# Kernel tuning notes

Hardware: AMD Instinct MI355X
Metric: run time of the kernel (lower is better)

The kernel has to match this reference:

```python
import jax, jax.numpy as jnp
import numpy as np
import math

S, B, D = 2048, 2, 1024
H = 16
DH = D // H
WIN = 256
DIL = 1


def setup_inputs() -> dict:
    key = jax.random.key(0)
    ks = jax.random.split(key, 10)
    std = 1.0 / math.sqrt(D)
    return {
        "x": jax.random.normal(ks[0], (S, B, D), jnp.float32),
        "beta": jax.random.normal(ks[1], (H,), jnp.float32) * 0.02,
        "Wq": jax.random.normal(ks[2], (D, D), jnp.float32) * std,
        "bq": jnp.zeros((D,), jnp.float32),
        "Wk": jax.random.normal(ks[3], (D, D), jnp.float32) * std,
        "bk": jnp.zeros((D,), jnp.float32),
        "Wv": jax.random.normal(ks[4], (D, D), jnp.float32) * std,
        "bv": jnp.zeros((D,), jnp.float32),
        "Wo": jax.random.normal(ks[5], (D, D), jnp.float32) * std,
        "bo": jnp.zeros((D,), jnp.float32),
    }


def _split_heads(t):
    # (S, B, D) -> (B*H, S, DH), matching rearrange 's b (h d) -> (b h) s d'
    return t.reshape(S, B, H, DH).transpose(1, 2, 0, 3).reshape(B * H, S, DH)


def reference(x, beta, Wq, bq, Wk, bk, Wv, bv, Wo, bo):
    q = _split_heads(x @ Wq + bq)
    k = _split_heads(x @ Wk + bk)
    v = _split_heads(x @ Wv + bv)

    # per-head learnable temperature: q / (sqrt(d_head) * exp(beta))
    beta_exp = jnp.tile(jnp.exp(beta), B)  # (B*H,), head index = z % H
    q = q / (jnp.sqrt(jnp.asarray(DH, x.dtype)) * beta_exp)[:, None, None]

    # causal dilated windowed mask
    idx = jnp.arange(S)
    diff = idx[:, None] - idx[None, :]
    allowed = (diff >= 0) & (diff <= DIL * (WIN - 1)) & (diff % DIL == 0)
    mask = jnp.where(allowed, jnp.asarray(0.0, x.dtype), jnp.asarray(-jnp.inf, x.dtype))

    scores = jnp.einsum('zqd,zkd->zqk', q, k) + mask[None]
    # attention sink: extra zero-logit column absorbing probability mass
    scores = jnp.concatenate([scores, jnp.zeros((B * H, S, 1), scores.dtype)], axis=-1)
    attn = jax.nn.softmax(scores, axis=-1)[..., :-1]

    out = jnp.einsum('zqk,zkd->zqd', attn, v)
    # (B*H, S, DH) -> (S, B, D)
    out = out.reshape(B, H, S, DH).transpose(2, 0, 1, 3).reshape(S, B, D)
    return out @ Wo + bo
```

## Files before the change

### kernel.cpp

```cpp
#include <hip/hip_runtime.h>
#include <math.h>

#define S_LEN  2048
#define BATCH  2
#define DM     1024
#define NHEAD  16
#define DHEAD  64
#define WIN    256
#define MROWS  4096

#define KP   72
#define PPAD 68

#define BM 256
#define BN 192
#define BK 64

typedef __attribute__((ext_vector_type(8))) short bf16x8;
typedef __attribute__((ext_vector_type(4))) float f32x4;

__device__ __forceinline__ unsigned short f2b(float f) {
    unsigned int u = __float_as_uint(f);
    return (unsigned short)((u + 0x7fffu + ((u >> 16) & 1u)) >> 16);
}
__device__ __forceinline__ void gld16(const void* g, void* l) {
    __builtin_amdgcn_global_load_lds(
        (const __attribute__((address_space(1))) void*)g,
        (__attribute__((address_space(3))) void*)l, 16, 0, 0);
}
__device__ __forceinline__ bf16x8 pack8(float4 a, float4 b) {
    bf16x8 r;
    r[0] = (short)f2b(a.x); r[1] = (short)f2b(a.y);
    r[2] = (short)f2b(a.z); r[3] = (short)f2b(a.w);
    r[4] = (short)f2b(b.x); r[5] = (short)f2b(b.y);
    r[6] = (short)f2b(b.z); r[7] = (short)f2b(b.w);
    return r;
}

__global__ __launch_bounds__(256)
void cvtx(const float* __restrict__ x, unsigned short* __restrict__ xb)
{
    const int i = (blockIdx.x * 256 + threadIdx.x) * 4;
    float4 f = *(const float4*)(x + i);
    ushort4 o; o.x = f2b(f.x); o.y = f2b(f.y); o.z = f2b(f.z); o.w = f2b(f.w);
    *(ushort4*)(xb + i) = o;
}

__global__ __launch_bounds__(256)
void twcvt4(const float* __restrict__ W0, const float* __restrict__ W1,
            const float* __restrict__ W2, const float* __restrict__ W3,
            unsigned short* __restrict__ T0, unsigned short* __restrict__ T1,
            unsigned short* __restrict__ T2, unsigned short* __restrict__ T3)
{
    const int zz = blockIdx.z;
    const float* W = (zz == 0) ? W0 : (zz == 1) ? W1 : (zz == 2) ? W2 : W3;
    unsigned short* WT = (zz == 0) ? T0 : (zz == 1) ? T1 : (zz == 2) ? T2 : T3;

    __shared__ float t32[32][33];
    const int bx = blockIdx.x * 32;
    const int by = blockIdx.y * 32;
    const int c  = threadIdx.x & 31;
    const int r0 = threadIdx.x >> 5;
#pragma unroll
    for (int p = 0; p < 4; ++p)
        t32[r0 + 8 * p][c] = W[(size_t)(by + r0 + 8 * p) * DM + bx + c];
    __syncthreads();
#pragma unroll
    for (int p = 0; p < 4; ++p)
        WT[(size_t)(bx + r0 + 8 * p) * DM + by + c] = f2b(t32[c][r0 + 8 * p]);
}

__global__ __launch_bounds__(512, 2)
void gemm_qkv(const unsigned short* __restrict__ A,
              const unsigned short* __restrict__ BT,
              const float* __restrict__ b0,
              const float* __restrict__ b1,
              const float* __restrict__ b2,
              const float* __restrict__ beta,
              unsigned short* __restrict__ Cb)
{
    __shared__ unsigned short Ab[2][BM * BK];
    __shared__ unsigned short Bb[2][BN * BK];

    const int t   = threadIdx.x;
    const int ln  = t & 63;
    const int wv  = t >> 6;
    const int wr  = wv >> 2;
    const int wc  = wv & 3;
    const int m16 = ln & 15;
    const int g   = ln >> 4;
    const int sw  = m16 & 7;

    const int rowBase = blockIdx.y * BM;
    const int colBase = blockIdx.x * BN;

    const int sr  = t >> 3;
    const int scx = (t & 7) ^ (sr & 7);
    const size_t gOff = (size_t)sr * DM + scx * 8;
    const int    ldOff = t * 8;

    f32x4 acc[8][3];
#pragma unroll
    for (int u = 0; u < 8; ++u)
#pragma unroll
        for (int v = 0; v < 3; ++v)
            acc[u][v] = (f32x4){0.f, 0.f, 0.f, 0.f};

    {
        const unsigned short* a0 = A  + (size_t)rowBase * DM + gOff;
        const unsigned short* bt = BT + (size_t)colBase * DM + gOff;
#pragma unroll
        for (int cb = 0; cb < 3; ++cb)
            gld16(bt + (size_t)cb * 64 * DM, &Bb[0][cb * 4096 + ldOff]);
#pragma unroll
        for (int ca = 0; ca < 4; ++ca)
            gld16(a0 + (size_t)ca * 64 * DM, &Ab[0][ca * 4096 + ldOff]);
        asm volatile("s_waitcnt vmcnt(0)" ::: "memory");
        __builtin_amdgcn_s_barrier();
    }

    bf16x8 af[4][2], bfr[2][2];

    for (int kt = 0; kt < DM / BK; ++kt) {
        const int cur = kt & 1;
        const unsigned short* Ac = Ab[cur];
        const unsigned short* Bc = Bb[cur];
        unsigned short* An = Ab[cur ^ 1];
        unsigned short* Bn = Bb[cur ^ 1];
        const bool hn = (kt < DM / BK - 1);
        const unsigned short* aS = A  + (size_t)rowBase * DM + (kt + 1) * BK + gOff;
        const unsigned short* bS = BT + (size_t)colBase * DM + (kt + 1) * BK + gOff;

#pragma unroll
        for (int u = 0; u < 4; ++u) {
            const int ro = (wr * 128 + u * 16 + m16) * BK;
#pragma unroll
            for (int kk = 0; kk < 2; ++kk)
                af[u][kk] = *(const bf16x8*)&Ac[ro + (((kk << 2) | g) ^ sw) * 8];
        }
#pragma unroll
        for (int v = 0; v < 2; ++v) {
            const int ro = (wc * 48 + v * 16 + m16) * BK;
#pragma unroll
            for (int kk = 0; kk < 2; ++kk)
                bfr[v][kk] = *(const bf16x8*)&Bc[ro + (((kk << 2) | g) ^ sw) * 8];
        }
        if (hn) {
            gld16(bS,                      &Bn[ldOff]);
            gld16(bS + (size_t)64 * DM,    &Bn[4096 + ldOff]);
        }
        __builtin_amdgcn_s_barrier();
        __builtin_amdgcn_s_setprio(1);
#pragma unroll
        for (int u = 0; u < 4; ++u)
#pragma unroll
            for (int v = 0; v < 2; ++v) {
                acc[u][v] = __builtin_amdgcn_mfma_f32_16x16x32_bf16(
                    af[u][0], bfr[v][0], acc[u][v], 0, 0, 0);
                acc[u][v] = __builtin_amdgcn_mfma_f32_16x16x32_bf16(
                    af[u][1], bfr[v][1], acc[u][v], 0, 0, 0);
            }
        __builtin_amdgcn_s_setprio(0);
        __builtin_amdgcn_s_barrier();

        {
            const int ro = (wc * 48 + 32 + m16) * BK;
#pragma unroll
            for (int kk = 0; kk < 2; ++kk)
                bfr[0][kk] = *(const bf16x8*)&Bc[ro + (((kk << 2) | g) ^ sw) * 8];
        }
        if (hn) {
            gld16(bS + (size_t)128 * DM,   &Bn[2 * 4096 + ldOff]);
            gld16(aS,                      &An[ldOff]);
        }
        __builtin_amdgcn_s_barrier();
        __builtin_amdgcn_s_setprio(1);
#pragma unroll
        for (int u = 0; u < 4; ++u) {
            acc[u][2] = __builtin_amdgcn_mfma_f32_16x16x32_bf16(
                af[u][0], bfr[0][0], acc[u][2], 0, 0, 0);
            acc[u][2] = __builtin_amdgcn_mfma_f32_16x16x32_bf16(
                af[u][1], bfr[0][1], acc[u][2], 0, 0, 0);
        }
        __builtin_amdgcn_s_setprio(0);
        asm volatile("s_waitcnt vmcnt(4)" ::: "memory");
        __builtin_amdgcn_s_barrier();

#pragma unroll
        for (int u = 0; u < 4; ++u) {
            const int ro = (wr * 128 + 64 + u * 16 + m16) * BK;
#pragma unroll
            for (int kk = 0; kk < 2; ++kk)
                af[u][kk] = *(const bf16x8*)&Ac[ro + (((kk << 2) | g) ^ sw) * 8];
        }
#pragma unroll
        for (int v = 0; v < 2; ++v) {
            const int ro = (wc * 48 + v * 16 + m16) * BK;
#pragma unroll
            for (int kk = 0; kk < 2; ++kk)
                bfr[v][kk] = *(const bf16x8*)&Bc[ro + (((kk << 2) | g) ^ sw) * 8];
        }
        if (hn) {
            gld16(aS + (size_t)128 * DM,   &An[2 * 4096 + ldOff]);
            gld16(aS + (size_t)64 * DM,    &An[4096 + ldOff]);
        }
        __builtin_amdgcn_s_barrier();
        __builtin_amdgcn_s_setprio(1);
#pragma unroll
        for (int u = 0; u < 4; ++u)
#pragma unroll
            for (int v = 0; v < 2; ++v) {
                acc[4 + u][v] = __builtin_amdgcn_mfma_f32_16x16x32_bf16(
                    af[u][0], bfr[v][0], acc[4 + u][v], 0, 0, 0);
                acc[4 + u][v] = __builtin_amdgcn_mfma_f32_16x16x32_bf16(
                    af[u][1], bfr[v][1], acc[4 + u][v], 0, 0, 0);
            }
        __builtin_amdgcn_s_setprio(0);
        __builtin_amdgcn_s_barrier();

        {
            const int ro = (wc * 48 + 32 + m16) * BK;
#pragma unroll
            for (int kk = 0; kk < 2; ++kk)
                bfr[0][kk] = *(const bf16x8*)&Bc[ro + (((kk << 2) | g) ^ sw) * 8];
        }
        if (hn) {
            gld16(aS + (size_t)192 * DM,   &An[3 * 4096 + ldOff]);
        }
        __builtin_amdgcn_s_barrier();
        __builtin_amdgcn_s_setprio(1);
#pragma unroll
        for (int u = 0; u < 4; ++u) {
            acc[4 + u][2] = __builtin_amdgcn_mfma_f32_16x16x32_bf16(
                af[u][0], bfr[0][0], acc[4 + u][2], 0, 0, 0);
            acc[4 + u][2] = __builtin_amdgcn_mfma_f32_16x16x32_bf16(
                af[u][1], bfr[0][1], acc[4 + u][2], 0, 0, 0);
        }
        __builtin_amdgcn_s_setprio(0);
        asm volatile("s_waitcnt vmcnt(2)" ::: "memory");
        __builtin_amdgcn_s_barrier();
    }

    const int q4 = g * 4;
#pragma unroll
    for (int v = 0; v < 3; ++v) {
        const int col = colBase + wc * 48 + v * 16 + m16;
        const int sec = col >> 10;
        const int h   = (col >> 6) & (NHEAD - 1);
        const int dh  = col & 63;
        if (sec < 2) {
            const float bi = (sec == 0 ? b0 : b1)[col & (DM - 1)];
            const float sc = (sec == 0) ? 0.125f * __expf(-beta[h]) : 1.0f;
            unsigned short* base = Cb + (size_t)sec * MROWS * DM;
#pragma unroll
            for (int u = 0; u < 8; ++u)
#pragma unroll
                for (int r = 0; r < 4; ++r) {
                    const int row = rowBase + wr * 128 + u * 16 + q4 + r;
                    const int s = row >> 1, bb = row & 1;
                    const int z = bb * NHEAD + h;
                    base[((size_t)z * S_LEN + s) * DHEAD + dh] =
                        f2b((acc[u][v][r] + bi) * sc);
                }
        } else {
            unsigned short* vtb = Cb + (size_t)2 * MROWS * DM;
            const float bi = b2[col & (DM - 1)];
#pragma unroll
            for (int u = 0; u < 8; ++u) {
                const int row0 = rowBase + wr * 128 + u * 16 + q4;
                const int s0   = row0 >> 1;
                ushort2 p0, p1;
                p0.x = f2b(acc[u][v][0] + bi);
                p0.y = f2b(acc[u][v][2] + bi);
                p1.x = f2b(acc[u][v][1] + bi);
                p1.y = f2b(acc[u][v][3] + bi);
                *(ushort2*)(vtb + ((size_t)(h * DHEAD + dh) * S_LEN + s0)) = p0;
                *(ushort2*)(vtb + ((size_t)((NHEAD + h) * DHEAD + dh) * S_LEN + s0)) = p1;
            }
        }
    }
}

__global__ __launch_bounds__(256)
void gemm_out(const unsigned short* __restrict__ A,
              const unsigned short* __restrict__ BT,
              const float* __restrict__ bias,
              float* __restrict__ Cf)
{
    __shared__ unsigned short As[128 * 32];
    __shared__ unsigned short Bs[64 * 32];

    const int t  = threadIdx.x;
    const int wv = t >> 6, ln = t & 63;
    const int rowBase = blockIdx.y * 128;
    const int colBase = blockIdx.x * 64;

    const int m16 = ln & 15, g = ln >> 4;
    const int wr = wv >> 1, wc = wv & 1;
    const int swz = (m16 >> 1) & 3;

    const int lr = ln >> 2;
    const int lq = (ln & 3) ^ ((lr >> 1) & 3);
    const unsigned short* ga = A  + (size_t)(rowBase + wv * 16 + lr) * DM + lq * 8;
    const unsigned short* gb = BT + (size_t)(colBase + wv * 16 + lr) * DM + lq * 8;
    unsigned short* la0 = As + wv * 512;
    unsigned short* la1 = la0 + 2048;
    unsigned short* lb  = Bs + wv * 512;

    f32x4 acc[4][2];
#pragma unroll
    for (int u = 0; u < 4; ++u)
#pragma unroll
        for (int v = 0; v < 2; ++v)
            acc[u][v] = (f32x4){0.f, 0.f, 0.f, 0.f};

    for (int kb = 0; kb < DM; kb += 32) {
        gld16(ga + kb, la0);
        gld16(ga + (size_t)64 * DM + kb, la1);
        gld16(gb + kb, lb);
        __syncthreads();

        bf16x8 af[4], bfr[2];
#pragma unroll
        for (int u = 0; u < 4; ++u)
            af[u] = *(const bf16x8*)&As[(wr * 64 + u * 16 + m16) * 32 + ((g ^ swz) * 8)];
#pragma unroll
        for (int v = 0; v < 2; ++v)
            bfr[v] = *(const bf16x8*)&Bs[(wc * 32 + v * 16 + m16) * 32 + ((g ^ swz) * 8)];
#pragma unroll
        for (int u = 0; u < 4; ++u)
#pragma unroll
            for (int v = 0; v < 2; ++v)
                acc[u][v] = __builtin_amdgcn_mfma_f32_16x16x32_bf16(
                    af[u], bfr[v], acc[u][v], 0, 0, 0);
        __syncthreads();
    }

    const int q4 = g * 4;
#pragma unroll
    for (int v = 0; v < 2; ++v) {
        const int col = colBase + wc * 32 + v * 16 + m16;
        const float bi = bias[col];
#pragma unroll
        for (int u = 0; u < 4; ++u)
#pragma unroll
            for (int r = 0; r < 4; ++r) {
                const int row = rowBase + wr * 64 + u * 16 + q4 + r;
                Cf[(size_t)row * DM + col] = acc[u][v][r] + bi;
            }
    }
}

__global__ __launch_bounds__(256, 4)
void attn_mfma(const unsigned short* __restrict__ q,
               const unsigned short* __restrict__ k,
               const unsigned short* __restrict__ vt,
               unsigned short* __restrict__ ao)
{
    __shared__ unsigned short Ks[64 * KP];
    __shared__ unsigned short Vs[64 * KP];
    __shared__ float Ps[64][PPAD];

    const int t   = threadIdx.x;
    const int wv  = t >> 6, ln = t & 63;
    const int m16 = ln & 15, g = ln >> 4;
    const int z   = blockIdx.y;
    const int q0  = blockIdx.x * 64;
    const size_t zbase = (size_t)z * S_LEN * DHEAD;

    const unsigned short* qrow = q + zbase + (size_t)(q0 + wv * 16 + m16) * DHEAD;
    bf16x8 qf0 = *(const bf16x8*)(qrow + g * 8);
    bf16x8 qf1 = *(const bf16x8*)(qrow + 32 + g * 8);

    f32x4 oacc[4];
#pragma unroll
    for (int v4 = 0; v4 < 4; ++v4) oacc[v4] = (f32x4){0.f, 0.f, 0.f, 0.f};
    float lr[4];
#pragma unroll
    for (int r = 0; r < 4; ++r) lr[r] = 1.f;

    for (int c = 0; c < 5; ++c) {
        const int kb = q0 - 256 + c * 64;
        if (kb < 0) continue;
        __syncthreads();

#pragma unroll
        for (int i = 0; i < 2; ++i) {
            const int id  = t + 256 * i;
            const int row = id >> 3;
            const int co  = (id & 7) * 8;
            *(bf16x8*)&Ks[row * KP + co] =
                *(const bf16x8*)(k + zbase + (size_t)(kb + row) * DHEAD + co);
            *(bf16x8*)&Vs[row * KP + co] =
                *(const bf16x8*)(vt + ((size_t)z * DHEAD + row) * S_LEN + kb + co);
        }
        __syncthreads();

        f32x4 sacc[4];
#pragma unroll
        for (int v4 = 0; v4 < 4; ++v4) {
            sacc[v4] = (f32x4){0.f, 0.f, 0.f, 0.f};
            bf16x8 kf0 = *(const bf16x8*)&Ks[(v4 * 16 + m16) * KP + g * 8];
            sacc[v4] = __builtin_amdgcn_mfma_f32_16x16x32_bf16(qf0, kf0, sacc[v4], 0, 0, 0);
            bf16x8 kf1 = *(const bf16x8*)&Ks[(v4 * 16 + m16) * KP + 32 + g * 8];
            sacc[v4] = __builtin_amdgcn_mfma_f32_16x16x32_bf16(qf1, kf1, sacc[v4], 0, 0, 0);
        }

        const bool mhi = (c == 4), mlo = (c == 0);
#pragma unroll
        for (int r = 0; r < 4; ++r) {
            const int ig = q0 + wv * 16 + g * 4 + r;
            float rsum = 0.f;
#pragma unroll
            for (int v4 = 0; v4 < 4; ++v4) {
                const int jg = kb + v4 * 16 + m16;
                float x = sacc[v4][r];
                const bool valid = (!mhi || jg <= ig) && (!mlo || jg >= ig - (WIN - 1));
                x = valid ? x : -1e30f;
                const float pp = __expf(x);
                Ps[wv * 16 + g * 4 + r][v4 * 16 + m16] = pp;
                rsum += pp;
            }
#pragma unroll
            for (int off = 1; off < 16; off <<= 1)
                rsum += __shfl_xor(rsum, off, 64);
            lr[r] += rsum;
        }
        __syncthreads();

        const float* prow = &Ps[wv * 16 + m16][0];
        bf16x8 pf0 = pack8(*(const float4*)(prow + g * 8),
                           *(const float4*)(prow + g * 8 + 4));
        bf16x8 pf1 = pack8(*(const float4*)(prow + 32 + g * 8),
                           *(const float4*)(prow + 32 + g * 8 + 4));
#pragma unroll
        for (int v4 = 0; v4 < 4; ++v4) {
            bf16x8 vf0 = *(const bf16x8*)&Vs[(v4 * 16 + m16) * KP + g * 8];
            oacc[v4] = __builtin_amdgcn_mfma_f32_16x16x32_bf16(pf0, vf0, oacc[v4], 0, 0, 0);
            bf16x8 vf1 = *(const bf16x8*)&Vs[(v4 * 16 + m16) * KP + 32 + g * 8];
            oacc[v4] = __builtin_amdgcn_mfma_f32_16x16x32_bf16(pf1, vf1, oacc[v4], 0, 0, 0);
        }
    }

    const int bb = z >> 4, h = z & 15;
#pragma unroll
    for (int r = 0; r < 4; ++r) {
        const int ig  = q0 + wv * 16 + g * 4 + r;
        const float inv = 1.f / lr[r];
#pragma unroll
        for (int v4 = 0; v4 < 4; ++v4)
            ao[(size_t)(ig * BATCH + bb) * DM + h * DHEAD + v4 * 16 + m16] =
                f2b(oacc[v4][r] * inv);
    }
}

extern "C" void kernel_launch(void* const* d_in, const int* in_sizes, int n_in,
                              void* d_out, int out_size, void* d_ws, size_t ws_size,
                              hipStream_t stream)
{
    const float* x    = (const float*)d_in[0];
    const float* beta = (const float*)d_in[1];
    const float* Wq   = (const float*)d_in[2];
    const float* bq   = (const float*)d_in[3];
    const float* Wk   = (const float*)d_in[4];
    const float* bk   = (const float*)d_in[5];
    const float* Wv   = (const float*)d_in[6];
    const float* bv   = (const float*)d_in[7];
    const float* Wo   = (const float*)d_in[8];
    const float* bo   = (const float*)d_in[9];
    float* out = (float*)d_out;

    unsigned short* w = (unsigned short*)d_ws;
    const size_t seg = (size_t)MROWS * DM;
    unsigned short* qb  = w;
    unsigned short* kb  = w + seg;
    unsigned short* vtb = w + 2 * seg;
    unsigned short* ab  = w + 3 * seg;
    unsigned short* xb  = w + 4 * seg;
    unsigned short* wtq = w + 5 * seg;
    unsigned short* wtk = wtq + (size_t)DM * DM;
    unsigned short* wtv = wtk + (size_t)DM * DM;
    unsigned short* wto = wtv + (size_t)DM * DM;

    cvtx<<<4096, 256, 0, stream>>>(x, xb);
    twcvt4<<<dim3(32, 32, 4), 256, 0, stream>>>(Wq, Wk, Wv, Wo, wtq, wtk, wtv, wto);

    gemm_qkv<<<dim3(3072 / BN, MROWS / BM), 512, 0, stream>>>(
        xb, wtq, bq, bk, bv, beta, qb);

    attn_mfma<<<dim3(S_LEN / 64, BATCH * NHEAD), 256, 0, stream>>>(qb, kb, vtb, ab);

    gemm_out<<<dim3(DM / 64, MROWS / 128), 256, 0, stream>>>(ab, wto, bo, out);
}
```

Baseline: 175.2 us.

## Simplify QKV GEMM pipeline and retile output GEMM with double-buffered 128x128 tiles

The QKV GEMM drops its four-phase interleaved schedule with many barriers. Each wave now computes a 64x96 tile, issues all next-tile global-to-LDS loads at once, and syncs once per K step. The output GEMM moves from a single-buffered 128x64 tile with BK=32 and two syncthreads per step to a double-buffered 128x128 tile with BK=64 and direct-to-LDS loads, cutting barrier count and raising reuse per byte loaded. The cost is less overlap granularity in the QKV kernel and fewer blocks in the output GEMM (256), which lowers parallelism on a large GPU.

```diff
diff --git a/kernel.cpp b/kernel.cpp
--- a/kernel.cpp
+++ b/kernel.cpp
@@ -15,6 +15,9 @@
 #define BM 256
 #define BN 192
 #define BK 64
+
+#define OM 128
+#define ON 128
 
 typedef __attribute__((ext_vector_type(8))) short bf16x8;
 typedef __attribute__((ext_vector_type(4))) float f32x4;
@@ -85,8 +88,8 @@
     const int t   = threadIdx.x;
     const int ln  = t & 63;
     const int wv  = t >> 6;
-    const int wr  = wv >> 2;
-    const int wc  = wv & 3;
+    const int wr  = wv & 3;
+    const int wc  = wv >> 2;
     const int m16 = ln & 15;
     const int g   = ln >> 4;
     const int sw  = m16 & 7;
@@ -99,11 +102,11 @@
     const size_t gOff = (size_t)sr * DM + scx * 8;
     const int    ldOff = t * 8;
 
-    f32x4 acc[8][3];
-#pragma unroll
-    for (int u = 0; u < 8; ++u)
-#pragma unroll
-        for (int v = 0; v < 3; ++v)
+    f32x4 acc[4][6];
+#pragma unroll
+    for (int u = 0; u < 4; ++u)
+#pragma unroll
+        for (int v = 0; v < 6; ++v)
             acc[u][v] = (f32x4){0.f, 0.f, 0.f, 0.f};
 
     {
@@ -117,9 +120,8 @@
             gld16(a0 + (size_t)ca * 64 * DM, &Ab[0][ca * 4096 + ldOff]);
         asm volatile("s_waitcnt vmcnt(0)" ::: "memory");
         __builtin_amdgcn_s_barrier();
-    }
-
-    bf16x8 af[4][2], bfr[2][2];
+        __builtin_amdgcn_sched_barrier(0);
+    }
 
     for (int kt = 0; kt < DM / BK; ++kt) {
         const int cur = kt & 1;
@@ -131,120 +133,60 @@
         const unsigned short* aS = A  + (size_t)rowBase * DM + (kt + 1) * BK + gOff;
         const unsigned short* bS = BT + (size_t)colBase * DM + (kt + 1) * BK + gOff;
 
-#pragma unroll
-        for (int u = 0; u < 4; ++u) {
-            const int ro = (wr * 128 + u * 16 + m16) * BK;
-#pragma unroll
-            for (int kk = 0; kk < 2; ++kk)
-                af[u][kk] = *(const bf16x8*)&Ac[ro + (((kk << 2) | g) ^ sw) * 8];
-        }
-#pragma unroll
-        for (int v = 0; v < 2; ++v) {
-            const int ro = (wc * 48 + v * 16 + m16) * BK;
-#pragma unroll
-            for (int kk = 0; kk < 2; ++kk)
-                bfr[v][kk] = *(const bf16x8*)&Bc[ro + (((kk << 2) | g) ^ sw) * 8];
-        }
+        bf16x8 af0[4], bf0[6];
+#pragma unroll
+        for (int u = 0; u < 4; ++u)
+            af0[u] = *(const bf16x8*)&Ac[(wr * 64 + u * 16 + m16) * BK + ((g ^ sw) * 8)];
+#pragma unroll
+        for (int v = 0; v < 6; ++v)
+            bf0[v] = *(const bf16x8*)&Bc[(wc * 96 + v * 16 + m16) * BK + ((g ^ sw) * 8)];
+
         if (hn) {
-            gld16(bS,                      &Bn[ldOff]);
-            gld16(bS + (size_t)64 * DM,    &Bn[4096 + ldOff]);
-        }
+            gld16(bS,                    &Bn[ldOff]);
+            gld16(bS + (size_t)64 * DM,  &Bn[4096 + ldOff]);
+            gld16(bS + (size_t)128 * DM, &Bn[2 * 4096 + ldOff]);
+            gld16(aS,                    &An[ldOff]);
+            gld16(aS + (size_t)64 * DM,  &An[4096 + ldOff]);
+            gld16(aS + (size_t)128 * DM, &An[2 * 4096 + ldOff]);
+            gld16(aS + (size_t)192 * DM, &An[3 * 4096 + ldOff]);
+        }
+
+        __builtin_amdgcn_s_setprio(1);
+#pragma unroll
+        for (int u = 0; u < 4; ++u)
+#pragma unroll
+            for (int v = 0; v < 6; ++v)
+                acc[u][v] = __builtin_amdgcn_mfma_f32_16x16x32_bf16(
+                    af0[u], bf0[v], acc[u][v], 0, 0, 0);
+        __builtin_amdgcn_s_setprio(0);
+
+        bf16x8 af1[4], bf1[6];
+#pragma unroll
+        for (int u = 0; u < 4; ++u)
+            af1[u] = *(const bf16x8*)&Ac[(wr * 64 + u * 16 + m16) * BK + (((4 | g) ^ sw) * 8)];
+#pragma unroll
+        for (int v = 0; v < 6; ++v)
+            bf1[v] = *(const bf16x8*)&Bc[(wc * 96 + v * 16 + m16) * BK + (((4 | g) ^ sw) * 8)];
+
+        __builtin_amdgcn_s_setprio(1);
+#pragma unroll
+        for (int u = 0; u < 4; ++u)
+#pragma unroll
+            for (int v = 0; v < 6; ++v)
+                acc[u][v] = __builtin_amdgcn_mfma_f32_16x16x32_bf16(
+                    af1[u], bf1[v], acc[u][v], 0, 0, 0);
+        __builtin_amdgcn_s_setprio(0);
+
+        if (hn)
+            asm volatile("s_waitcnt vmcnt(0)" ::: "memory");
         __builtin_amdgcn_s_barrier();
-        __builtin_amdgcn_s_setprio(1);
-#pragma unroll
-        for (int u = 0; u < 4; ++u)
-#pragma unroll
-            for (int v = 0; v < 2; ++v) {
-                acc[u][v] = __builtin_amdgcn_mfma_f32_16x16x32_bf16(
-                    af[u][0], bfr[v][0], acc[u][v], 0, 0, 0);
-                acc[u][v] = __builtin_amdgcn_mfma_f32_16x16x32_bf16(
-                    af[u][1], bfr[v][1], acc[u][v], 0, 0, 0);
-            }
-        __builtin_amdgcn_s_setprio(0);
-        __builtin_amdgcn_s_barrier();
-
-        {
-            const int ro = (wc * 48 + 32 + m16) * BK;
-#pragma unroll
-            for (int kk = 0; kk < 2; ++kk)
-                bfr[0][kk] = *(const bf16x8*)&Bc[ro + (((kk << 2) | g) ^ sw) * 8];
-        }
-        if (hn) {
-            gld16(bS + (size_t)128 * DM,   &Bn[2 * 4096 + ldOff]);
-            gld16(aS,                      &An[ldOff]);
-        }
-        __builtin_amdgcn_s_barrier();
-        __builtin_amdgcn_s_setprio(1);
-#pragma unroll
-        for (int u = 0; u < 4; ++u) {
-            acc[u][2] = __builtin_amdgcn_mfma_f32_16x16x32_bf16(
-                af[u][0], bfr[0][0], acc[u][2], 0, 0, 0);
-            acc[u][2] = __builtin_amdgcn_mfma_f32_16x16x32_bf16(
-                af[u][1], bfr[0][1], acc[u][2], 0, 0, 0);
-        }
-        __builtin_amdgcn_s_setprio(0);
-        asm volatile("s_waitcnt vmcnt(4)" ::: "memory");
-        __builtin_amdgcn_s_barrier();
-
-#pragma unroll
-        for (int u = 0; u < 4; ++u) {
-            const int ro = (wr * 128 + 64 + u * 16 + m16) * BK;
-#pragma unroll
-            for (int kk = 0; kk < 2; ++kk)
-                af[u][kk] = *(const bf16x8*)&Ac[ro + (((kk << 2) | g) ^ sw) * 8];
-        }
-#pragma unroll
-        for (int v = 0; v < 2; ++v) {
-            const int ro = (wc * 48 + v * 16 + m16) * BK;
-#pragma unroll
-            for (int kk = 0; kk < 2; ++kk)
-                bfr[v][kk] = *(const bf16x8*)&Bc[ro + (((kk << 2) | g) ^ sw) * 8];
-        }
-        if (hn) {
-            gld16(aS + (size_t)128 * DM,   &An[2 * 4096 + ldOff]);
-            gld16(aS + (size_t)64 * DM,    &An[4096 + ldOff]);
-        }
-        __builtin_amdgcn_s_barrier();
-        __builtin_amdgcn_s_setprio(1);
-#pragma unroll
-        for (int u = 0; u < 4; ++u)
-#pragma unroll
-            for (int v = 0; v < 2; ++v) {
-                acc[4 + u][v] = __builtin_amdgcn_mfma_f32_16x16x32_bf16(
-                    af[u][0], bfr[v][0], acc[4 + u][v], 0, 0, 0);
-                acc[4 + u][v] = __builtin_amdgcn_mfma_f32_16x16x32_bf16(
-                    af[u][1], bfr[v][1], acc[4 + u][v], 0, 0, 0);
-            }
-        __builtin_amdgcn_s_setprio(0);
-        __builtin_amdgcn_s_barrier();
-
-        {
-            const int ro = (wc * 48 + 32 + m16) * BK;
-#pragma unroll
-            for (int kk = 0; kk < 2; ++kk)
-                bfr[0][kk] = *(const bf16x8*)&Bc[ro + (((kk << 2) | g) ^ sw) * 8];
-        }
-        if (hn) {
-            gld16(aS + (size_t)192 * DM,   &An[3 * 4096 + ldOff]);
-        }
-        __builtin_amdgcn_s_barrier();
-        __builtin_amdgcn_s_setprio(1);
-#pragma unroll
-        for (int u = 0; u < 4; ++u) {
-            acc[4 + u][2] = __builtin_amdgcn_mfma_f32_16x16x32_bf16(
-                af[u][0], bfr[0][0], acc[4 + u][2], 0, 0, 0);
-            acc[4 + u][2] = __builtin_amdgcn_mfma_f32_16x16x32_bf16(
-                af[u][1], bfr[0][1], acc[4 + u][2], 0, 0, 0);
-        }
-        __builtin_amdgcn_s_setprio(0);
-        asm volatile("s_waitcnt vmcnt(2)" ::: "memory");
-        __builtin_amdgcn_s_barrier();
+        __builtin_amdgcn_sched_barrier(0);
     }
 
     const int q4 = g * 4;
 #pragma unroll
-    for (int v = 0; v < 3; ++v) {
-        const int col = colBase + wc * 48 + v * 16 + m16;
+    for (int v = 0; v < 6; ++v) {
+        const int col = colBase + wc * 96 + v * 16 + m16;
         const int sec = col >> 10;
         const int h   = (col >> 6) & (NHEAD - 1);
         const int dh  = col & 63;
@@ -253,10 +195,10 @@
             const float sc = (sec == 0) ? 0.125f * __expf(-beta[h]) : 1.0f;
             unsigned short* base = Cb + (size_t)sec * MROWS * DM;
 #pragma unroll
-            for (int u = 0; u < 8; ++u)
+            for (int u = 0; u < 4; ++u)
 #pragma unroll
                 for (int r = 0; r < 4; ++r) {
-                    const int row = rowBase + wr * 128 + u * 16 + q4 + r;
+                    const int row = rowBase + wr * 64 + u * 16 + q4 + r;
                     const int s = row >> 1, bb = row & 1;
                     const int z = bb * NHEAD + h;
                     base[((size_t)z * S_LEN + s) * DHEAD + dh] =
@@ -266,8 +208,8 @@
             unsigned short* vtb = Cb + (size_t)2 * MROWS * DM;
             const float bi = b2[col & (DM - 1)];
 #pragma unroll
-            for (int u = 0; u < 8; ++u) {
-                const int row0 = rowBase + wr * 128 + u * 16 + q4;
+            for (int u = 0; u < 4; ++u) {
+                const int row0 = rowBase + wr * 64 + u * 16 + q4;
                 const int s0   = row0 >> 1;
                 ushort2 p0, p1;
                 p0.x = f2b(acc[u][v][0] + bi);
@@ -281,65 +223,125 @@
     }
 }
 
-__global__ __launch_bounds__(256)
+__global__ __launch_bounds__(256, 2)
 void gemm_out(const unsigned short* __restrict__ A,
               const unsigned short* __restrict__ BT,
               const float* __restrict__ bias,
               float* __restrict__ Cf)
 {
-    __shared__ unsigned short As[128 * 32];
-    __shared__ unsigned short Bs[64 * 32];
+    __shared__ unsigned short As[2][OM * BK];
+    __shared__ unsigned short Bs[2][ON * BK];
 
     const int t  = threadIdx.x;
     const int wv = t >> 6, ln = t & 63;
-    const int rowBase = blockIdx.y * 128;
-    const int colBase = blockIdx.x * 64;
-
+    const int wr = wv >> 1, wc = wv & 1;
     const int m16 = ln & 15, g = ln >> 4;
-    const int wr = wv >> 1, wc = wv & 1;
-    const int swz = (m16 >> 1) & 3;
-
-    const int lr = ln >> 2;
-    const int lq = (ln & 3) ^ ((lr >> 1) & 3);
-    const unsigned short* ga = A  + (size_t)(rowBase + wv * 16 + lr) * DM + lq * 8;
-    const unsigned short* gb = BT + (size_t)(colBase + wv * 16 + lr) * DM + lq * 8;
-    unsigned short* la0 = As + wv * 512;
-    unsigned short* la1 = la0 + 2048;
-    unsigned short* lb  = Bs + wv * 512;
-
-    f32x4 acc[4][2];
+    const int sw  = m16 & 7;
+
+    const int rowBase = blockIdx.y * OM;
+    const int colBase = blockIdx.x * ON;
+
+    const int sr  = t >> 3;
+    const int scx = (t & 7) ^ (sr & 7);
+    const size_t gOff = (size_t)sr * DM + scx * 8;
+    const int    ldOff = t * 8;
+
+    f32x4 acc[4][4];
 #pragma unroll
     for (int u = 0; u < 4; ++u)
 #pragma unroll
-        for (int v = 0; v < 2; ++v)
+        for (int v = 0; v < 4; ++v)
             acc[u][v] = (f32x4){0.f, 0.f, 0.f, 0.f};
 
-    for (int kb = 0; kb < DM; kb += 32) {
-        gld16(ga + kb, la0);
-        gld16(ga + (size_t)64 * DM + kb, la1);
-        gld16(gb + kb, lb);
-        __syncthreads();
-
-        bf16x8 af[4], bfr[2];
-#pragma unroll
-        for (int u = 0; u < 4; ++u)
-            af[u] = *(const bf16x8*)&As[(wr * 64 + u * 16 + m16) * 32 + ((g ^ swz) * 8)];
-#pragma unroll
-        for (int v = 0; v < 2; ++v)
-            bfr[v] = *(const bf16x8*)&Bs[(wc * 32 + v * 16 + m16) * 32 + ((g ^ swz) * 8)];
-#pragma unroll
-        for (int u = 0; u < 4; ++u)
-#pragma unroll
-            for (int v = 0; v < 2; ++v)
+    {
+        const unsigned short* a0 = A  + (size_t)rowBase * DM + gOff;
+        const unsigned short* bt = BT + (size_t)colBase * DM + gOff;
+#pragma unroll
+        for (int ca = 0; ca < 2; ++ca)
+#pragma unroll
+            for (int hf = 0; hf < 2; ++hf)
+                gld16(a0 + (size_t)(ca * 64 + hf * 32) * DM,
+                      &As[0][ca * 4096 + hf * 2048 + ldOff]);
+#pragma unroll
+        for (int cb = 0; cb < 2; ++cb)
+#pragma unroll
+            for (int hf = 0; hf < 2; ++hf)
+                gld16(bt + (size_t)(cb * 64 + hf * 32) * DM,
+                      &Bs[0][cb * 4096 + hf * 2048 + ldOff]);
+        asm volatile("s_waitcnt vmcnt(0)" ::: "memory");
+        __builtin_amdgcn_s_barrier();
+        __builtin_amdgcn_sched_barrier(0);
+    }
+
+    for (int kt = 0; kt < DM / BK; ++kt) {
+        const int cur = kt & 1;
+        const unsigned short* Ac = As[cur];
+        const unsigned short* Bc = Bs[cur];
+        unsigned short* An = As[cur ^ 1];
+        unsigned short* Bn = Bs[cur ^ 1];
+        const bool hn = (kt < DM / BK - 1);
+        const unsigned short* aS = A  + (size_t)rowBase * DM + (kt + 1) * BK + gOff;
+        const unsigned short* bS = BT + (size_t)colBase * DM + (kt + 1) * BK + gOff;
+
+        bf16x8 af0[4], bf0[4];
+#pragma unroll
+        for (int u = 0; u < 4; ++u)
+            af0[u] = *(const bf16x8*)&Ac[(wr * 64 + u * 16 + m16) * BK + ((g ^ sw) * 8)];
+#pragma unroll
+        for (int v = 0; v < 4; ++v)
+            bf0[v] = *(const bf16x8*)&Bc[(wc * 64 + v * 16 + m16) * BK + ((g ^ sw) * 8)];
+
+        if (hn) {
+#pragma unroll
+            for (int ca = 0; ca < 2; ++ca)
+#pragma unroll
+                for (int hf = 0; hf < 2; ++hf)
+                    gld16(aS + (size_t)(ca * 64 + hf * 32) * DM,
+                          &An[ca * 4096 + hf * 2048 + ldOff]);
+#pragma unroll
+            for (int cb = 0; cb < 2; ++cb)
+#pragma unroll
+                for (int hf = 0; hf < 2; ++hf)
+                    gld16(bS + (size_t)(cb * 64 + hf * 32) * DM,
+                          &Bn[cb * 4096 + hf * 2048 + ldOff]);
+        }
+
+        __builtin_amdgcn_s_setprio(1);
+#pragma unroll
+        for (int u = 0; u < 4; ++u)
+#pragma unroll
+            for (int v = 0; v < 4; ++v)
                 acc[u][v] = __builtin_amdgcn_mfma_f32_16x16x32_bf16(
-                    af[u], bfr[v], acc[u][v], 0, 0, 0);
-        __syncthreads();
+                    af0[u], bf0[v], acc[u][v], 0, 0, 0);
+        __builtin_amdgcn_s_setprio(0);
+
+        bf16x8 af1[4], bf1[4];
+#pragma unroll
+        for (int u = 0; u < 4; ++u)
+            af1[u] = *(const bf16x8*)&Ac[(wr * 64 + u * 16 + m16) * BK + (((4 | g) ^ sw) * 8)];
+#pragma unroll
+        for (int v = 0; v < 4; ++v)
+            bf1[v] = *(const bf16x8*)&Bc[(wc * 64 + v * 16 + m16) * BK + (((4 | g) ^ sw) * 8)];
+
+        __builtin_amdgcn_s_setprio(1);
+#pragma unroll
+        for (int u = 0; u < 4; ++u)
+#pragma unroll
+            for (int v = 0; v < 4; ++v)
+                acc[u][v] = __builtin_amdgcn_mfma_f32_16x16x32_bf16(
+                    af1[u], bf1[v], acc[u][v], 0, 0, 0);
+        __builtin_amdgcn_s_setprio(0);
+
+        if (hn)
+            asm volatile("s_waitcnt vmcnt(0)" ::: "memory");
+        __builtin_amdgcn_s_barrier();
+        __builtin_amdgcn_sched_barrier(0);
     }
 
     const int q4 = g * 4;
 #pragma unroll
-    for (int v = 0; v < 2; ++v) {
-        const int col = colBase + wc * 32 + v * 16 + m16;
+    for (int v = 0; v < 4; ++v) {
+        const int col = colBase + wc * 64 + v * 16 + m16;
         const float bi = bias[col];
 #pragma unroll
         for (int u = 0; u < 4; ++u)
@@ -490,5 +492,5 @@
 
     attn_mfma<<<dim3(S_LEN / 64, BATCH * NHEAD), 256, 0, stream>>>(qb, kb, vtb, ab);
 
-    gemm_out<<<dim3(DM / 64, MROWS / 128), 256, 0, stream>>>(ab, wto, bo, out);
-}
+    gemm_out<<<dim3(DM / ON, MROWS / OM), 256, 0, stream>>>(ab, wto, bo, out);
+}
```

New measurement: 169.4 us. 1.03x faster.
